# Kernel tuning notes

Measured on AMD Instinct MI355X. Metric: run time of the kernel, lower is better.

The kernel has to match this reference:

```python
import jax, jax.numpy as jnp
import numpy as np

DIM = 2048
N_HEADS = 16
N_KV_HEADS = 8
HEAD_DIM = DIM // N_HEADS  # 128
N_REP = N_HEADS // N_KV_HEADS  # 2
B, L = 2, 2048
ROPE_THETA = 10000.0


def make_freqs_cis(L, head_dim, theta):
    inv = 1.0 / (theta ** (np.arange(0, head_dim, 2, dtype=np.float32) / head_dim))
    t = np.arange(L, dtype=np.float32)
    ang = np.outer(t, inv)  # [L, head_dim//2]
    return jnp.asarray(np.stack([np.cos(ang), np.sin(ang)], axis=-1))  # [L, hd//2, 2]


def setup_inputs() -> dict:
    key = jax.random.key(0)
    ks = jax.random.split(key, 5)
    s = 1.0 / np.sqrt(DIM)
    return {
        "x": jax.random.normal(ks[0], (B, L, DIM), dtype=jnp.float32),
        "freqs_cis": make_freqs_cis(L, HEAD_DIM, ROPE_THETA),
        "wq": jax.random.normal(ks[1], (DIM, N_HEADS * HEAD_DIM), dtype=jnp.float32) * s,
        "wk": jax.random.normal(ks[2], (DIM, N_KV_HEADS * HEAD_DIM), dtype=jnp.float32) * s,
        "wv": jax.random.normal(ks[3], (DIM, N_KV_HEADS * HEAD_DIM), dtype=jnp.float32) * s,
        "wo": jax.random.normal(ks[4], (N_HEADS * HEAD_DIM, DIM), dtype=jnp.float32) * s,
    }


def apply_rotary(x, freqs_cis):
    # x: [B, L, H, D]; freqs_cis: [L, D//2, 2] (cos, sin)
    xr = x.reshape(*x.shape[:-1], -1, 2)  # [B,L,H,D//2,2]
    cos = freqs_cis[None, :, None, :, 0]
    sin = freqs_cis[None, :, None, :, 1]
    out_r = xr[..., 0] * cos - xr[..., 1] * sin
    out_i = xr[..., 0] * sin + xr[..., 1] * cos
    return jnp.stack([out_r, out_i], axis=-1).reshape(x.shape).astype(x.dtype)


def reference(x, freqs_cis, wq, wk, wv, wo):
    Bx, Lx, _ = x.shape
    xq = (x @ wq).reshape(Bx, Lx, N_HEADS, HEAD_DIM)
    xk = (x @ wk).reshape(Bx, Lx, N_KV_HEADS, HEAD_DIM)
    xv = (x @ wv).reshape(Bx, Lx, N_KV_HEADS, HEAD_DIM)
    xq = apply_rotary(xq, freqs_cis)
    xk = apply_rotary(xk, freqs_cis)
    # repeat kv heads (GQA) then put heads first: [B, H, L, D]
    keys = jnp.repeat(xk, N_REP, axis=2).transpose(0, 2, 1, 3)
    values = jnp.repeat(xv, N_REP, axis=2).transpose(0, 2, 1, 3)
    xq = xq.transpose(0, 2, 1, 3)
    scores = jnp.einsum("bhqd,bhkd->bhqk", xq, keys) / jnp.sqrt(
        jnp.asarray(HEAD_DIM, dtype=xq.dtype))
    causal = jnp.tril(jnp.ones((Lx, Lx), dtype=bool))
    scores = jnp.where(causal[None, None], scores, -jnp.inf)
    probs = jax.nn.softmax(scores.astype(jnp.float32), axis=-1).astype(xq.dtype)
    out = jnp.einsum("bhqk,bhkd->bhqd", probs, values)
    out = out.transpose(0, 2, 1, 3).reshape(Bx, Lx, -1)
    return out @ wo
```

## Files before the change

### kernel.cpp

```cpp
#include <hip/hip_runtime.h>
#include <math.h>

typedef unsigned short u16;
typedef unsigned int   u32;
typedef u16   u16x8 __attribute__((ext_vector_type(8)));
typedef u16   u16x4 __attribute__((ext_vector_type(4)));
typedef u16   u16x2 __attribute__((ext_vector_type(2)));
typedef __bf16 bf16x8 __attribute__((ext_vector_type(8)));
typedef float  f32x4 __attribute__((ext_vector_type(4)));

__device__ __forceinline__ u16 f2b(float f) {
    union { float f; u32 u; } v; v.f = f;
    u32 u = v.u;
    return (u16)((u + 0x7FFFu + ((u >> 16) & 1u)) >> 16);
}

__device__ __forceinline__ void glds16(const void* g, void* l) {
    __builtin_amdgcn_global_load_lds(
        (__attribute__((address_space(1))) void*)(void*)g,
        (__attribute__((address_space(3))) void*)l, 16, 0, 0);
}

__global__ __launch_bounds__(256) void convert_f32_bf16(
    const float* __restrict__ src, u16* __restrict__ dst)
{
    const size_t i = ((size_t)blockIdx.x * 256 + threadIdx.x) * 8;
    f32x4 a = *(const f32x4*)&src[i];
    f32x4 b = *(const f32x4*)&src[i + 4];
    u16x8 o;
    #pragma unroll
    for (int j = 0; j < 4; ++j) { o[j] = f2b(a[j]); o[4 + j] = f2b(b[j]); }
    *(u16x8*)&dst[i] = o;
}

__global__ __launch_bounds__(256) void transpose_f32_bf16(
    const float* __restrict__ src, u16* __restrict__ dst, int R, int C)
{
    __shared__ u16 tile[64 * 72];
    const int t = threadIdx.x;
    const int r0 = blockIdx.y * 64, c0 = blockIdx.x * 64;
    #pragma unroll
    for (int i = 0; i < 2; ++i) {
        int idx = i * 256 + t;
        int r = idx >> 3, c8 = (idx & 7) * 8;
        const float* sp = &src[(size_t)(r0 + r) * C + c0 + c8];
        f32x4 a = *(const f32x4*)sp;
        f32x4 b = *(const f32x4*)(sp + 4);
        u16x8 v;
        #pragma unroll
        for (int j = 0; j < 4; ++j) { v[j] = f2b(a[j]); v[4 + j] = f2b(b[j]); }
        *(u16x8*)&tile[r * 72 + c8] = v;
    }
    __syncthreads();
    #pragma unroll
    for (int i = 0; i < 2; ++i) {
        int idx = i * 256 + t;
        int orow = idx >> 3, oc8 = (idx & 7) * 8;
        u16x8 w;
        #pragma unroll
        for (int j = 0; j < 8; ++j) w[j] = tile[(oc8 + j) * 72 + orow];
        *(u16x8*)&dst[(size_t)(c0 + orow) * R + r0 + oc8] = w;
    }
}

template <int MODE>
__global__ __launch_bounds__(256) void gemm_bt(
    const u16* __restrict__ A, const u16* __restrict__ Bt,
    u16* __restrict__ D0, u16* __restrict__ D1, u16* __restrict__ D2,
    float* __restrict__ Fout, const float* __restrict__ fc)
{
    __shared__ u16 SA[3 * 4096];
    __shared__ u16 SB[3 * 4096];
    const int t = threadIdx.x;
    const int wid = t >> 6, lane = t & 63;
    const int l15 = lane & 15, qd = lane >> 4;
    const int row0 = blockIdx.y * 128, col0 = blockIdx.x * 128;
    const int wm = (wid >> 1) * 64, wn = (wid & 1) * 64;

    const int sm = lane >> 2;
    const int sk = (lane & 3) * 8;
    const int c0 = wid * 2;
    const u16* Ag0 = A  + (size_t)(row0 + c0 * 16 + sm) * 2048 + sk;
    const u16* Ag1 = A  + (size_t)(row0 + (c0 + 1) * 16 + sm) * 2048 + sk;
    const u16* Bg0 = Bt + (size_t)(col0 + c0 * 16 + sm) * 2048 + sk;
    const u16* Bg1 = Bt + (size_t)(col0 + (c0 + 1) * 16 + sm) * 2048 + sk;
    const int lo0 = c0 * 512, lo1 = (c0 + 1) * 512;

    u16 *pa0 = SA, *pa1 = SA + 4096, *pa2 = SA + 8192;
    u16 *pb0 = SB, *pb1 = SB + 4096, *pb2 = SB + 8192;

    f32x4 acc[4][4] = {};

    glds16(Ag0, pa0 + lo0); glds16(Ag1, pa0 + lo1);
    glds16(Bg0, pb0 + lo0); glds16(Bg1, pb0 + lo1);
    glds16(Ag0 + 32, pa1 + lo0); glds16(Ag1 + 32, pa1 + lo1);
    glds16(Bg0 + 32, pb1 + lo0); glds16(Bg1 + 32, pb1 + lo1);
    asm volatile("s_waitcnt vmcnt(4)" ::: "memory");
    __builtin_amdgcn_s_barrier();

    for (int kt = 0; kt < 64; ++kt) {
        if (kt < 62) {
            const int ko = (kt + 2) * 32;
            glds16(Ag0 + ko, pa2 + lo0); glds16(Ag1 + ko, pa2 + lo1);
            glds16(Bg0 + ko, pb2 + lo0); glds16(Bg1 + ko, pb2 + lo1);
        }
        bf16x8 af[4], bfr[4];
        #pragma unroll
        for (int mt = 0; mt < 4; ++mt)
            af[mt] = *(const bf16x8*)&pa0[(wm + mt * 16 + l15) * 32 + qd * 8];
        #pragma unroll
        for (int nt = 0; nt < 4; ++nt)
            bfr[nt] = *(const bf16x8*)&pb0[(wn + nt * 16 + l15) * 32 + qd * 8];
        #pragma unroll
        for (int mt = 0; mt < 4; ++mt)
            #pragma unroll
            for (int nt = 0; nt < 4; ++nt)
                acc[mt][nt] = __builtin_amdgcn_mfma_f32_16x16x32_bf16(
                    af[mt], bfr[nt], acc[mt][nt], 0, 0, 0);
        if (kt < 62)
            asm volatile("s_waitcnt vmcnt(4)" ::: "memory");
        else if (kt == 62)
            asm volatile("s_waitcnt vmcnt(0)" ::: "memory");
        if (kt < 63) __builtin_amdgcn_s_barrier();
        u16* ta = pa0; pa0 = pa1; pa1 = pa2; pa2 = ta;
        u16* tb = pb0; pb0 = pb1; pb1 = pb2; pb2 = tb;
    }

    #pragma unroll
    for (int mt = 0; mt < 4; ++mt)
        #pragma unroll
        for (int nt = 0; nt < 4; ++nt) {
            const int gcol = col0 + wn + nt * 16 + l15;
            const int grow0 = row0 + wm + mt * 16 + qd * 4;
            if (MODE == 1) {
                #pragma unroll
                for (int r = 0; r < 4; ++r)
                    Fout[(size_t)(grow0 + r) * 2048 + gcol] = acc[mt][nt][r];
            } else if (gcol >= 3072) {
                const int vcol = gcol - 3072;
                const int vrow = vcol + (grow0 >> 11) * 1024;
                u16x4 v;
                #pragma unroll
                for (int r = 0; r < 4; ++r) v[r] = f2b(acc[mt][nt][r]);
                *(u16x4*)&D2[(size_t)vrow * 2048 + (grow0 & 2047)] = v;
            } else {
                const int p2 = gcol & 126;
                #pragma unroll
                for (int r = 0; r < 4; ++r) {
                    const int l = (grow0 + r) & 2047;
                    const float c = fc[l * 128 + p2];
                    const float s = fc[l * 128 + p2 + 1];
                    const float own = acc[mt][nt][r];
                    const float oth = __shfl_xor(own, 1);
                    const float rot = (l15 & 1) ? (oth * s + own * c)
                                                : (own * c - oth * s);
                    const u16 v = f2b(rot);
                    if (gcol < 2048)
                        D0[(size_t)(grow0 + r) * 2048 + gcol] = v;
                    else
                        D1[(size_t)(grow0 + r) * 1024 + (gcol - 2048)] = v;
                }
            }
        }
}

__global__ __launch_bounds__(256, 2) void attn_kernel(
    const u16* __restrict__ Q, const u16* __restrict__ K,
    const u16* __restrict__ Vt, u16* __restrict__ AO)
{
    __shared__ u16 SM[32768];
    const int t = threadIdx.x;
    const int w = t >> 6, lane = t & 63;
    const int l15 = lane & 15, qd = lane >> 4;
    const int b = blockIdx.x >> 3, kvh = blockIdx.x & 7;
    const int y = (int)blockIdx.y;
    const int qt = (y < 16) ? (31 - y) : (y - 16);
    const int h = kvh * 2 + (w >> 1);
    const float SCL = 0.08838834764831845f * 1.4426950408889634f;

    u16* K0 = SM;
    u16* K1 = SM + 8192;
    u16* VB = SM + 16384;
    u16* PW = SM + 24576 + w * 2048;

    bf16x8 qf[2][4];
    #pragma unroll
    for (int mt = 0; mt < 2; ++mt) {
        const size_t grow = (size_t)b * 2048 + qt * 64 + (w & 1) * 32 + mt * 16 + l15;
        const u16* qp = Q + grow * 2048 + h * 128 + qd * 8;
        #pragma unroll
        for (int ks = 0; ks < 4; ++ks)
            qf[mt][ks] = *(const bf16x8*)(qp + ks * 32);
    }
    f32x4 Oa[2][8] = {};
    f32x4 Ls[2] = {};
    bf16x8 onesv;
    #pragma unroll
    for (int j = 0; j < 8; ++j) onesv[j] = (__bf16)1.0f;

    const u16* Kbase = K  + (size_t)b * 2048 * 1024 + kvh * 128;
    const u16* Vbase = Vt + (size_t)(b * 8 + kvh) * 128 * 2048;

    #pragma unroll
    for (int j = 0; j < 4; ++j) {
        const int f = w * 4 + j;
        glds16(Kbase + (size_t)((f >> 2) * 16 + l15) * 1024 + ((f & 3) * 4 + qd) * 8,
               K0 + f * 512);
    }
    __syncthreads();

    for (int kt = 0; kt <= qt; ++kt) {
        u16* Kc = (kt & 1) ? K1 : K0;
        u16* Kn = (kt & 1) ? K0 : K1;
        if (kt < qt) {
            #pragma unroll
            for (int j = 0; j < 4; ++j) {
                const int f = w * 4 + j;
                glds16(Kbase + (size_t)((kt + 1) * 64 + (f >> 2) * 16 + l15) * 1024
                             + ((f & 3) * 4 + qd) * 8,
                       Kn + f * 512);
            }
        }
        #pragma unroll
        for (int j = 0; j < 4; ++j) {
            const int f = w * 4 + j;
            glds16(Vbase + (size_t)((f >> 1) * 16 + l15) * 2048 + kt * 64
                         + ((f & 1) * 4 + qd) * 8,
                   VB + f * 512);
        }

        f32x4 S[2][4] = {};
        #pragma unroll
        for (int ks = 0; ks < 4; ++ks) {
            bf16x8 bk[4];
            #pragma unroll
            for (int nt = 0; nt < 4; ++nt)
                bk[nt] = *(const bf16x8*)&Kc[(nt * 4 + ks) * 512 + lane * 8];
            __builtin_amdgcn_s_setprio(1);
            #pragma unroll
            for (int mt = 0; mt < 2; ++mt)
                #pragma unroll
                for (int nt = 0; nt < 4; ++nt)
                    S[mt][nt] = __builtin_amdgcn_mfma_f32_16x16x32_bf16(
                        qf[mt][ks], bk[nt], S[mt][nt], 0, 0, 0);
            __builtin_amdgcn_s_setprio(0);
        }
        if (kt == qt) {
            #pragma unroll
            for (int mt = 0; mt < 2; ++mt)
                #pragma unroll
                for (int r = 0; r < 4; ++r) {
                    const int qg = (w & 1) * 32 + mt * 16 + qd * 4 + r;
                    #pragma unroll
                    for (int nt = 0; nt < 4; ++nt)
                        if (nt * 16 + l15 > qg) S[mt][nt][r] = -__builtin_inff();
                }
        }
        #pragma unroll
        for (int mt = 0; mt < 2; ++mt)
            #pragma unroll
            for (int nt = 0; nt < 4; ++nt)
                #pragma unroll
                for (int r = 0; r < 4; ++r) {
                    const float p = exp2f(S[mt][nt][r] * SCL - 12.0f);
                    PW[(mt * 2 + (nt >> 1)) * 512 + ((nt * 2 + (l15 >> 3)) & 3) * 128
                       + (qd * 4 + r) * 8 + (l15 & 7)] = f2b(p);
                }

        __syncthreads();

        #pragma unroll
        for (int ks = 0; ks < 2; ++ks) {
            bf16x8 pa[2], vb[8];
            #pragma unroll
            for (int mt = 0; mt < 2; ++mt)
                pa[mt] = *(const bf16x8*)&PW[(mt * 2 + ks) * 512 + lane * 8];
            #pragma unroll
            for (int nt = 0; nt < 8; ++nt)
                vb[nt] = *(const bf16x8*)&VB[(nt * 2 + ks) * 512 + lane * 8];
            __builtin_amdgcn_s_setprio(1);
            #pragma unroll
            for (int mt = 0; mt < 2; ++mt) {
                Ls[mt] = __builtin_amdgcn_mfma_f32_16x16x32_bf16(
                    pa[mt], onesv, Ls[mt], 0, 0, 0);
                #pragma unroll
                for (int nt = 0; nt < 8; ++nt)
                    Oa[mt][nt] = __builtin_amdgcn_mfma_f32_16x16x32_bf16(
                        pa[mt], vb[nt], Oa[mt][nt], 0, 0, 0);
            }
            __builtin_amdgcn_s_setprio(0);
        }
        __syncthreads();
    }

    u16* OL = SM;
    #pragma unroll
    for (int mt = 0; mt < 2; ++mt)
        #pragma unroll
        for (int r = 0; r < 4; ++r) {
            const float inv = 1.f / Ls[mt][r];
            const int qr = (w & 1) * 32 + mt * 16 + qd * 4 + r;
            #pragma unroll
            for (int nt = 0; nt < 8; ++nt)
                OL[qr * 256 + (w >> 1) * 128 + nt * 16 + l15] = f2b(Oa[mt][nt][r] * inv);
        }
    __syncthreads();
    #pragma unroll
    for (int i = 0; i < 8; ++i) {
        const int c = i * 256 + t;
        const int row = c >> 5, ch = c & 31;
        u16x8 v = *(const u16x8*)&OL[row * 256 + ch * 8];
        *(u16x8*)&AO[((size_t)b * 2048 + qt * 64 + row) * 2048 + kvh * 256 + ch * 8] = v;
    }
}

extern "C" void kernel_launch(void* const* d_in, const int* in_sizes, int n_in,
                              void* d_out, int out_size, void* d_ws, size_t ws_size,
                              hipStream_t stream)
{
    (void)in_sizes; (void)n_in; (void)out_size; (void)ws_size;
    const float* x  = (const float*)d_in[0];
    const float* fc = (const float*)d_in[1];
    const float* wq = (const float*)d_in[2];
    const float* wk = (const float*)d_in[3];
    const float* wv = (const float*)d_in[4];
    const float* wo = (const float*)d_in[5];
    float* out = (float*)d_out;
    char* ws = (char*)d_ws;

    u16* Qb  = (u16*)(ws);
    u16* Kb  = (u16*)(ws + 16777216);
    u16* Vt  = (u16*)(ws + 25165824);
    u16* Xb  = (u16*)(ws + 33554432);
    u16* AO  = (u16*)(ws + 33554432);
    u16* WT  = (u16*)(ws + 50331648);
    u16* WOT = (u16*)(ws + 67108864);

    convert_f32_bf16<<<4096, 256, 0, stream>>>(x, Xb);
    transpose_f32_bf16<<<dim3(32, 32), 256, 0, stream>>>(wq, WT, 2048, 2048);
    transpose_f32_bf16<<<dim3(16, 32), 256, 0, stream>>>(wk, WT + 2048 * 2048, 2048, 1024);
    transpose_f32_bf16<<<dim3(16, 32), 256, 0, stream>>>(wv, WT + 3072 * 2048, 2048, 1024);
    transpose_f32_bf16<<<dim3(32, 32), 256, 0, stream>>>(wo, WOT, 2048, 2048);

    gemm_bt<0><<<dim3(32, 32), 256, 0, stream>>>(Xb, WT, Qb, Kb, Vt, nullptr, fc);

    attn_kernel<<<dim3(16, 32), 256, 0, stream>>>(Qb, Kb, Vt, AO);

    gemm_bt<1><<<dim3(16, 32), 256, 0, stream>>>(AO, WOT, nullptr, nullptr, nullptr, out, nullptr);
}
```

Measured before the change: 270.8 us.

## Enlarge GEMM tiles to 256x256 with 8 waves and fragment-ordered LDS layout

The projection GEMMs move from 128x128 tiles with 4 waves to 256x256 tiles with 8 waves. Each wave now computes 128x64 outputs, so more MFMAs are issued per LDS fragment load and each block does more arithmetic per global byte. The LDS staging layout also changes so every lane loads its MFMA fragment contiguously (lane*8), which is meant to avoid bank conflicts. In exchange, the grids are much smaller (256 and 128 blocks), which can leave CUs idle on a 256-CU part, and register pressure rises with 32 accumulators per wave.

```diff
diff --git a/kernel.cpp b/kernel.cpp
--- a/kernel.cpp
+++ b/kernel.cpp
@@ -64,55 +64,53 @@
 }
 
 template <int MODE>
-__global__ __launch_bounds__(256) void gemm_bt(
+__global__ __launch_bounds__(512, 2) void gemm_bt(
     const u16* __restrict__ A, const u16* __restrict__ Bt,
     u16* __restrict__ D0, u16* __restrict__ D1, u16* __restrict__ D2,
     float* __restrict__ Fout, const float* __restrict__ fc)
 {
-    __shared__ u16 SA[3 * 4096];
-    __shared__ u16 SB[3 * 4096];
+    __shared__ u16 SA[3 * 8192];
+    __shared__ u16 SB[3 * 8192];
     const int t = threadIdx.x;
-    const int wid = t >> 6, lane = t & 63;
+    const int w = t >> 6, lane = t & 63;
     const int l15 = lane & 15, qd = lane >> 4;
-    const int row0 = blockIdx.y * 128, col0 = blockIdx.x * 128;
-    const int wm = (wid >> 1) * 64, wn = (wid & 1) * 64;
-
-    const int sm = lane >> 2;
-    const int sk = (lane & 3) * 8;
-    const int c0 = wid * 2;
-    const u16* Ag0 = A  + (size_t)(row0 + c0 * 16 + sm) * 2048 + sk;
-    const u16* Ag1 = A  + (size_t)(row0 + (c0 + 1) * 16 + sm) * 2048 + sk;
-    const u16* Bg0 = Bt + (size_t)(col0 + c0 * 16 + sm) * 2048 + sk;
-    const u16* Bg1 = Bt + (size_t)(col0 + (c0 + 1) * 16 + sm) * 2048 + sk;
-    const int lo0 = c0 * 512, lo1 = (c0 + 1) * 512;
-
-    u16 *pa0 = SA, *pa1 = SA + 4096, *pa2 = SA + 8192;
-    u16 *pb0 = SB, *pb1 = SB + 4096, *pb2 = SB + 8192;
-
-    f32x4 acc[4][4] = {};
-
-    glds16(Ag0, pa0 + lo0); glds16(Ag1, pa0 + lo1);
-    glds16(Bg0, pb0 + lo0); glds16(Bg1, pb0 + lo1);
-    glds16(Ag0 + 32, pa1 + lo0); glds16(Ag1 + 32, pa1 + lo1);
-    glds16(Bg0 + 32, pb1 + lo0); glds16(Bg1 + 32, pb1 + lo1);
+    const int row0 = blockIdx.y * 256, col0 = blockIdx.x * 256;
+    const int wmf = (w >> 2) * 8;
+    const int wnf = (w & 3) * 4;
+
+    const u16* Ag0 = A  + (size_t)(row0 + (w * 2 + 0) * 16 + l15) * 2048 + qd * 8;
+    const u16* Ag1 = A  + (size_t)(row0 + (w * 2 + 1) * 16 + l15) * 2048 + qd * 8;
+    const u16* Bg0 = Bt + (size_t)(col0 + (w * 2 + 0) * 16 + l15) * 2048 + qd * 8;
+    const u16* Bg1 = Bt + (size_t)(col0 + (w * 2 + 1) * 16 + l15) * 2048 + qd * 8;
+    const int fo0 = (w * 2 + 0) * 512, fo1 = (w * 2 + 1) * 512;
+
+    u16 *a0 = SA, *a1 = SA + 8192, *a2 = SA + 16384;
+    u16 *b0 = SB, *b1 = SB + 8192, *b2 = SB + 16384;
+
+    f32x4 acc[8][4] = {};
+
+    glds16(Ag0, a0 + fo0); glds16(Ag1, a0 + fo1);
+    glds16(Bg0, b0 + fo0); glds16(Bg1, b0 + fo1);
+    glds16(Ag0 + 32, a1 + fo0); glds16(Ag1 + 32, a1 + fo1);
+    glds16(Bg0 + 32, b1 + fo0); glds16(Bg1 + 32, b1 + fo1);
     asm volatile("s_waitcnt vmcnt(4)" ::: "memory");
     __builtin_amdgcn_s_barrier();
 
     for (int kt = 0; kt < 64; ++kt) {
         if (kt < 62) {
             const int ko = (kt + 2) * 32;
-            glds16(Ag0 + ko, pa2 + lo0); glds16(Ag1 + ko, pa2 + lo1);
-            glds16(Bg0 + ko, pb2 + lo0); glds16(Bg1 + ko, pb2 + lo1);
-        }
-        bf16x8 af[4], bfr[4];
-        #pragma unroll
-        for (int mt = 0; mt < 4; ++mt)
-            af[mt] = *(const bf16x8*)&pa0[(wm + mt * 16 + l15) * 32 + qd * 8];
+            glds16(Ag0 + ko, a2 + fo0); glds16(Ag1 + ko, a2 + fo1);
+            glds16(Bg0 + ko, b2 + fo0); glds16(Bg1 + ko, b2 + fo1);
+        }
+        bf16x8 af[8], bfr[4];
+        #pragma unroll
+        for (int mt = 0; mt < 8; ++mt)
+            af[mt] = *(const bf16x8*)&a0[(wmf + mt) * 512 + lane * 8];
         #pragma unroll
         for (int nt = 0; nt < 4; ++nt)
-            bfr[nt] = *(const bf16x8*)&pb0[(wn + nt * 16 + l15) * 32 + qd * 8];
-        #pragma unroll
-        for (int mt = 0; mt < 4; ++mt)
+            bfr[nt] = *(const bf16x8*)&b0[(wnf + nt) * 512 + lane * 8];
+        #pragma unroll
+        for (int mt = 0; mt < 8; ++mt)
             #pragma unroll
             for (int nt = 0; nt < 4; ++nt)
                 acc[mt][nt] = __builtin_amdgcn_mfma_f32_16x16x32_bf16(
@@ -122,16 +120,16 @@
         else if (kt == 62)
             asm volatile("s_waitcnt vmcnt(0)" ::: "memory");
         if (kt < 63) __builtin_amdgcn_s_barrier();
-        u16* ta = pa0; pa0 = pa1; pa1 = pa2; pa2 = ta;
-        u16* tb = pb0; pb0 = pb1; pb1 = pb2; pb2 = tb;
-    }
-
-    #pragma unroll
-    for (int mt = 0; mt < 4; ++mt)
+        u16* ta = a0; a0 = a1; a1 = a2; a2 = ta;
+        u16* tb = b0; b0 = b1; b1 = b2; b2 = tb;
+    }
+
+    #pragma unroll
+    for (int mt = 0; mt < 8; ++mt)
         #pragma unroll
         for (int nt = 0; nt < 4; ++nt) {
-            const int gcol = col0 + wn + nt * 16 + l15;
-            const int grow0 = row0 + wm + mt * 16 + qd * 4;
+            const int gcol = col0 + (w & 3) * 64 + nt * 16 + l15;
+            const int grow0 = row0 + (w >> 2) * 128 + mt * 16 + qd * 4;
             if (MODE == 1) {
                 #pragma unroll
                 for (int r = 0; r < 4; ++r)
@@ -342,9 +340,9 @@
     transpose_f32_bf16<<<dim3(16, 32), 256, 0, stream>>>(wv, WT + 3072 * 2048, 2048, 1024);
     transpose_f32_bf16<<<dim3(32, 32), 256, 0, stream>>>(wo, WOT, 2048, 2048);
 
-    gemm_bt<0><<<dim3(32, 32), 256, 0, stream>>>(Xb, WT, Qb, Kb, Vt, nullptr, fc);
+    gemm_bt<0><<<dim3(16, 16), 512, 0, stream>>>(Xb, WT, Qb, Kb, Vt, nullptr, fc);
 
     attn_kernel<<<dim3(16, 32), 256, 0, stream>>>(Qb, Kb, Vt, AO);
 
-    gemm_bt<1><<<dim3(16, 32), 256, 0, stream>>>(AO, WOT, nullptr, nullptr, nullptr, out, nullptr);
-}
+    gemm_bt<1><<<dim3(8, 16), 512, 0, stream>>>(AO, WOT, nullptr, nullptr, nullptr, out, nullptr);
+}
```

New measurement: 334.4 us. 1.24x slower.
